# Kernel tuning notes

Measured on AMD Instinct MI355X. Metric: run time of the kernel, lower is better.

## Reference

```python
import jax, jax.numpy as jnp
import numpy as np

B, IN, H = 4096, 1024, 1024


def setup_inputs() -> dict:
    key = jax.random.key(0)
    k1, k2, k3, k4 = jax.random.split(key, 4)
    x = jax.random.normal(k1, (B, IN), dtype=jnp.float32)
    h_prev = jax.random.normal(k2, (B, H), dtype=jnp.float32)
    c_prev = jax.random.normal(k3, (B, H), dtype=jnp.float32)
    # Kaiming-uniform-ish init for W: bound = sqrt(6 / fan_in)
    fan_in = IN + H
    bound = np.sqrt(6.0 / fan_in)
    W = jax.random.uniform(k4, (4 * H, IN + H), dtype=jnp.float32,
                           minval=-bound, maxval=bound)
    # bias zero except forget-gate bias = 1.0 (first H entries)
    b = jnp.zeros((4 * H,), dtype=jnp.float32).at[:H].set(1.0)
    return {"x": x, "h_prev": h_prev, "c_prev": c_prev, "W": W, "b": b}


def reference(x, h_prev, c_prev, W, b):
    Hdim = c_prev.shape[1]
    combined = jnp.concatenate([x, h_prev], axis=1)        # (B, IN+H)
    gates = combined @ W.T + b                             # (B, 4H)
    f = jax.nn.sigmoid(gates[:, :Hdim])
    i = jax.nn.sigmoid(gates[:, Hdim:2 * Hdim])
    g = jnp.tanh(gates[:, 2 * Hdim:3 * Hdim])
    o = jax.nn.sigmoid(gates[:, 3 * Hdim:])
    c_t = f * c_prev + i * g
    h_t = o * jnp.tanh(c_t)
    return (h_t, c_t)
```

## Files before the change

### kernel.cpp

```cpp
#include <hip/hip_runtime.h>
#include <stdint.h>

#define Bn 4096
#define INn 1024
#define Hn 1024
#define Kn 2048
#define Nn 4096

#define BM 128
#define BK 64

typedef __attribute__((ext_vector_type(8))) short bf16x8;
typedef __attribute__((ext_vector_type(4))) float f32x4;
typedef __attribute__((ext_vector_type(4))) unsigned short us4;

__device__ __forceinline__ unsigned short f2bf(float f) {
  uint32_t u = __float_as_uint(f);
  u += 0x7fffu + ((u >> 16) & 1u);
  return (unsigned short)(u >> 16);
}

typedef __attribute__((address_space(3))) unsigned int as3_uint;
typedef const __attribute__((address_space(1))) unsigned int as1_uint;

__device__ __forceinline__ void gload16(const unsigned short* g, unsigned short* l) {
  __builtin_amdgcn_global_load_lds((as1_uint*)g, (as3_uint*)l, 16, 0, 0);
}

__device__ __forceinline__ float sigm(float x) { return 1.f / (1.f + __expf(-x)); }
__device__ __forceinline__ float tanh_fast(float x) { return 2.f / (1.f + __expf(-2.f * x)) - 1.f; }

__global__ void pack_bf16(const float* __restrict__ src, unsigned short* __restrict__ dst,
                          int log2cols, int dst_stride, int dst_col_off, long nquads) {
  long stride = (long)gridDim.x * blockDim.x;
  for (long q = (long)blockIdx.x * blockDim.x + threadIdx.x; q < nquads; q += stride) {
    long e = q << 2;
    int row = (int)(e >> log2cols);
    int col = (int)(e & ((1L << log2cols) - 1));
    float4 v = *(const float4*)(src + e);
    us4 o;
    o.x = f2bf(v.x); o.y = f2bf(v.y); o.z = f2bf(v.z); o.w = f2bf(v.w);
    *(us4*)(dst + (long)row * dst_stride + dst_col_off + col) = o;
  }
}

__global__ void lstm_gemm_fused(const unsigned short* __restrict__ A,
                                const unsigned short* __restrict__ Wbf,
                                const float* __restrict__ c_prev,
                                const float* __restrict__ bias,
                                float* __restrict__ out) {
  __shared__ unsigned short As[BM * BK];
  __shared__ unsigned short Bs[BM * BK];
  const int tid = threadIdx.x;
  const int lane = tid & 63;
  const int wid = tid >> 6;
  const int wr = wid >> 1;
  const int wc = wid & 1;
  const int brow = blockIdx.y * BM;
  const int h0 = blockIdx.x * 32;

  const int srow = tid >> 3;
  const int skoff = (tid & 7) * 8;

  const int l15 = lane & 15;
  const int lk = (lane >> 4) * 8;

  f32x4 acc[4][4] = {};

  for (int kt = 0; kt < Kn / BK; ++kt) {
    const int k0 = kt * BK;
#pragma unroll
    for (int i = 0; i < 4; ++i) {
      gload16(A + (long)(brow + i * 32 + srow) * Kn + k0 + skoff,
              &As[(i * 32 + srow) * BK + skoff]);
      const int rb = i * 32 + srow;
      const int grow = ((rb >> 4) & 3) * 1024 + h0 + ((rb >> 6) << 4) + (rb & 15);
      gload16(Wbf + (long)grow * Kn + k0 + skoff,
              &Bs[rb * BK + skoff]);
    }
    __syncthreads();
#pragma unroll
    for (int ks = 0; ks < 2; ++ks) {
      bf16x8 af[4], bfr[4];
#pragma unroll
      for (int m = 0; m < 4; ++m)
        af[m] = *(const bf16x8*)&As[(wr * 64 + m * 16 + l15) * BK + ks * 32 + lk];
#pragma unroll
      for (int n = 0; n < 4; ++n)
        bfr[n] = *(const bf16x8*)&Bs[(wc * 64 + n * 16 + l15) * BK + ks * 32 + lk];
#pragma unroll
      for (int m = 0; m < 4; ++m)
#pragma unroll
        for (int n = 0; n < 4; ++n)
          acc[m][n] = __builtin_amdgcn_mfma_f32_16x16x32_bf16(af[m], bfr[n], acc[m][n], 0, 0, 0);
    }
    __syncthreads();
  }

  const int hcol = h0 + wc * 16 + l15;
  const float bf_ = bias[hcol];
  const float bi_ = bias[1024 + hcol];
  const float bg_ = bias[2048 + hcol];
  const float bo_ = bias[3072 + hcol];
  const int rbase = brow + wr * 64 + ((lane >> 4) << 2);
  const long BH = (long)Bn * Hn;
#pragma unroll
  for (int m = 0; m < 4; ++m) {
#pragma unroll
    for (int j = 0; j < 4; ++j) {
      const long r = rbase + m * 16 + j;
      const float f = sigm(acc[m][0][j] + bf_);
      const float i_ = sigm(acc[m][1][j] + bi_);
      const float g = tanh_fast(acc[m][2][j] + bg_);
      const float o = sigm(acc[m][3][j] + bo_);
      const float cp = c_prev[r * Hn + hcol];
      const float ct = f * cp + i_ * g;
      const float ht = o * tanh_fast(ct);
      out[r * Hn + hcol] = ht;
      out[BH + r * Hn + hcol] = ct;
    }
  }
}

extern "C" void kernel_launch(void* const* d_in, const int* in_sizes, int n_in,
                              void* d_out, int out_size, void* d_ws, size_t ws_size,
                              hipStream_t stream) {
  const float* x      = (const float*)d_in[0];
  const float* h_prev = (const float*)d_in[1];
  const float* c_prev = (const float*)d_in[2];
  const float* W      = (const float*)d_in[3];
  const float* bias   = (const float*)d_in[4];
  float* out = (float*)d_out;

  unsigned short* Abf = (unsigned short*)d_ws;
  unsigned short* Wbf = Abf + (long)Bn * Kn;

  pack_bf16<<<2048, 256, 0, stream>>>(x, Abf, 10, Kn, 0, (long)Bn * INn / 4);
  pack_bf16<<<2048, 256, 0, stream>>>(h_prev, Abf, 10, Kn, INn, (long)Bn * Hn / 4);
  pack_bf16<<<2048, 256, 0, stream>>>(W, Wbf, 11, Kn, 0, (long)Nn * Kn / 4);

  dim3 grid(Hn / 32, Bn / BM);
  lstm_gemm_fused<<<grid, 256, 0, stream>>>(Abf, Wbf, c_prev, bias, out);
}
```

Before: 204.5 us.

## Triple-buffer GEMM with swizzled LDS, larger tile, and single fused pack kernel

Merges the three bf16 pack launches into one kernel. Rewrites the GEMM main loop to use a 3-stage LDS ring with async global-to-LDS loads and explicit vmcnt waits, so tile fetches overlap the MFMA work. It also XOR-swizzles the LDS layout to avoid bank conflicts, and doubles the N tile to 64 hidden columns with 512-thread blocks. Split barriers and s_setprio interleave loads with MFMAs, at the cost of more LDS per block and hand-tuned wait counts that must match the number of outstanding loads.

```diff
diff --git a/kernel.cpp b/kernel.cpp
--- a/kernel.cpp
+++ b/kernel.cpp
@@ -8,7 +8,9 @@
 #define Nn 4096
 
 #define BM 128
+#define BN 256
 #define BK 64
+#define KT (Kn / BK)
 
 typedef __attribute__((ext_vector_type(8))) short bf16x8;
 typedef __attribute__((ext_vector_type(4))) float f32x4;
@@ -30,78 +32,149 @@
 __device__ __forceinline__ float sigm(float x) { return 1.f / (1.f + __expf(-x)); }
 __device__ __forceinline__ float tanh_fast(float x) { return 2.f / (1.f + __expf(-2.f * x)) - 1.f; }
 
-__global__ void pack_bf16(const float* __restrict__ src, unsigned short* __restrict__ dst,
-                          int log2cols, int dst_stride, int dst_col_off, long nquads) {
-  long stride = (long)gridDim.x * blockDim.x;
-  for (long q = (long)blockIdx.x * blockDim.x + threadIdx.x; q < nquads; q += stride) {
-    long e = q << 2;
-    int row = (int)(e >> log2cols);
-    int col = (int)(e & ((1L << log2cols) - 1));
-    float4 v = *(const float4*)(src + e);
+__global__ void pack_all(const float* __restrict__ x, const float* __restrict__ h,
+                         const float* __restrict__ W,
+                         unsigned short* __restrict__ Abf, unsigned short* __restrict__ Wbf) {
+  const long XQ = (long)Bn * INn / 4;
+  const long WQ = (long)Nn * Kn / 4;
+  const long total = XQ + XQ + WQ;
+  const long stride = (long)gridDim.x * blockDim.x;
+  for (long q = (long)blockIdx.x * blockDim.x + threadIdx.x; q < total; q += stride) {
+    float4 v;
+    unsigned short* dst;
+    if (q < XQ) {
+      long e = q << 2;
+      v = *(const float4*)(x + e);
+      dst = Abf + ((long)(e >> 10) * Kn) + (e & 1023);
+    } else if (q < 2 * XQ) {
+      long e = (q - XQ) << 2;
+      v = *(const float4*)(h + e);
+      dst = Abf + ((long)(e >> 10) * Kn) + INn + (e & 1023);
+    } else {
+      long e = (q - 2 * XQ) << 2;
+      v = *(const float4*)(W + e);
+      dst = Wbf + e;
+    }
     us4 o;
     o.x = f2bf(v.x); o.y = f2bf(v.y); o.z = f2bf(v.z); o.w = f2bf(v.w);
-    *(us4*)(dst + (long)row * dst_stride + dst_col_off + col) = o;
+    *(us4*)dst = o;
   }
 }
 
-__global__ void lstm_gemm_fused(const unsigned short* __restrict__ A,
-                                const unsigned short* __restrict__ Wbf,
-                                const float* __restrict__ c_prev,
-                                const float* __restrict__ bias,
-                                float* __restrict__ out) {
-  __shared__ unsigned short As[BM * BK];
-  __shared__ unsigned short Bs[BM * BK];
+#define STAGE_A(t_, b_) do {                                                     \
+    const int k0_ = (t_) * BK;                                                   \
+    gload16(Ag + (long)(brow + srow) * Kn + k0_ + scol,                          \
+            &bufA[b_][srow * BK + sc8 * 8]);                                     \
+    gload16(Ag + (long)(brow + 64 + srow) * Kn + k0_ + scol,                     \
+            &bufA[b_][(64 + srow) * BK + sc8 * 8]);                              \
+  } while (0)
+#define STAGE_B(t_, b_, j_) do {                                                 \
+    const int k0_ = (t_) * BK;                                                   \
+    const int rb_ = (j_) * 64 + srow;                                            \
+    const int grow_ = ((rb_ >> 4) & 3) * Hn + h0 + ((rb_ >> 6) << 4) + (rb_ & 15);\
+    gload16(Wg + (long)grow_ * Kn + k0_ + scol,                                  \
+            &bufB[b_][rb_ * BK + sc8 * 8]);                                      \
+  } while (0)
+#define FENCE() do { asm volatile("" ::: "memory"); __builtin_amdgcn_sched_barrier(0); } while (0)
+
+__global__ void __launch_bounds__(512, 2)
+lstm_gemm_fused(const unsigned short* __restrict__ Ag,
+                const unsigned short* __restrict__ Wg,
+                const float* __restrict__ c_prev,
+                const float* __restrict__ bias,
+                float* __restrict__ out) {
+  __shared__ unsigned short bufA[3][BM * BK];
+  __shared__ unsigned short bufB[3][BN * BK];
+
   const int tid = threadIdx.x;
   const int lane = tid & 63;
   const int wid = tid >> 6;
-  const int wr = wid >> 1;
-  const int wc = wid & 1;
+  const int wr = wid >> 2;
+  const int wc = wid & 3;
   const int brow = blockIdx.y * BM;
-  const int h0 = blockIdx.x * 32;
+  const int h0 = blockIdx.x * 64;
 
   const int srow = tid >> 3;
-  const int skoff = (tid & 7) * 8;
+  const int sc8 = tid & 7;
+  const int scol = ((sc8 ^ (srow & 7)) * 8);
 
   const int l15 = lane & 15;
-  const int lk = (lane >> 4) * 8;
+  const int s7 = l15 & 7;
+  const int cA = lane >> 4;
+  const int aOff0 = (wr * 64 + l15) * BK + ((cA) ^ s7) * 8;
+  const int aOff1 = (wr * 64 + l15) * BK + ((cA + 4) ^ s7) * 8;
+  const int bOff0 = (wc * 64 + l15) * BK + ((cA) ^ s7) * 8;
+  const int bOff1 = (wc * 64 + l15) * BK + ((cA + 4) ^ s7) * 8;
 
   f32x4 acc[4][4] = {};
 
-  for (int kt = 0; kt < Kn / BK; ++kt) {
-    const int k0 = kt * BK;
-#pragma unroll
-    for (int i = 0; i < 4; ++i) {
-      gload16(A + (long)(brow + i * 32 + srow) * Kn + k0 + skoff,
-              &As[(i * 32 + srow) * BK + skoff]);
-      const int rb = i * 32 + srow;
-      const int grow = ((rb >> 4) & 3) * 1024 + h0 + ((rb >> 6) << 4) + (rb & 15);
-      gload16(Wbf + (long)grow * Kn + k0 + skoff,
-              &Bs[rb * BK + skoff]);
-    }
-    __syncthreads();
-#pragma unroll
-    for (int ks = 0; ks < 2; ++ks) {
-      bf16x8 af[4], bfr[4];
-#pragma unroll
-      for (int m = 0; m < 4; ++m)
-        af[m] = *(const bf16x8*)&As[(wr * 64 + m * 16 + l15) * BK + ks * 32 + lk];
-#pragma unroll
-      for (int n = 0; n < 4; ++n)
-        bfr[n] = *(const bf16x8*)&Bs[(wc * 64 + n * 16 + l15) * BK + ks * 32 + lk];
-#pragma unroll
-      for (int m = 0; m < 4; ++m)
-#pragma unroll
-        for (int n = 0; n < 4; ++n)
-          acc[m][n] = __builtin_amdgcn_mfma_f32_16x16x32_bf16(af[m], bfr[n], acc[m][n], 0, 0, 0);
-    }
-    __syncthreads();
+  STAGE_A(0, 0); STAGE_B(0, 0, 0); STAGE_B(0, 0, 1); STAGE_B(0, 0, 2); STAGE_B(0, 0, 3);
+  STAGE_A(1, 1); STAGE_B(1, 1, 0); STAGE_B(1, 1, 1); STAGE_B(1, 1, 2); STAGE_B(1, 1, 3);
+
+  for (int t = 0; t < KT; ++t) {
+    const int bi = t % 3;
+    const int sb = (t + 2) % 3;
+    const bool st = (t + 2) < KT;
+    if (t < KT - 1) asm volatile("s_waitcnt vmcnt(6)" ::: "memory");
+    else            asm volatile("s_waitcnt vmcnt(0)" ::: "memory");
+    __builtin_amdgcn_s_barrier();
+    FENCE();
+
+    const unsigned short* As = bufA[bi];
+    const unsigned short* Bs = bufB[bi];
+    bf16x8 bfr[4][2], af[2][2];
+
+#pragma unroll
+    for (int n = 0; n < 4; ++n) {
+      bfr[n][0] = *(const bf16x8*)&Bs[bOff0 + n * 16 * BK];
+      bfr[n][1] = *(const bf16x8*)&Bs[bOff1 + n * 16 * BK];
+    }
+#pragma unroll
+    for (int m = 0; m < 2; ++m) {
+      af[m][0] = *(const bf16x8*)&As[aOff0 + m * 16 * BK];
+      af[m][1] = *(const bf16x8*)&As[aOff1 + m * 16 * BK];
+    }
+    if (st) { STAGE_A(t + 2, sb); STAGE_B(t + 2, sb, 0); }
+    __builtin_amdgcn_s_barrier();
+    FENCE();
+    __builtin_amdgcn_s_setprio(1);
+#pragma unroll
+    for (int m = 0; m < 2; ++m)
+#pragma unroll
+      for (int n = 0; n < 4; ++n) {
+        acc[m][n] = __builtin_amdgcn_mfma_f32_16x16x32_bf16(af[m][0], bfr[n][0], acc[m][n], 0, 0, 0);
+        acc[m][n] = __builtin_amdgcn_mfma_f32_16x16x32_bf16(af[m][1], bfr[n][1], acc[m][n], 0, 0, 0);
+      }
+    __builtin_amdgcn_s_setprio(0);
+    FENCE();
+    __builtin_amdgcn_s_barrier();
+    FENCE();
+
+#pragma unroll
+    for (int m = 0; m < 2; ++m) {
+      af[m][0] = *(const bf16x8*)&As[aOff0 + (m + 2) * 16 * BK];
+      af[m][1] = *(const bf16x8*)&As[aOff1 + (m + 2) * 16 * BK];
+    }
+    if (st) { STAGE_B(t + 2, sb, 1); STAGE_B(t + 2, sb, 2); STAGE_B(t + 2, sb, 3); }
+    __builtin_amdgcn_s_barrier();
+    FENCE();
+    __builtin_amdgcn_s_setprio(1);
+#pragma unroll
+    for (int m = 0; m < 2; ++m)
+#pragma unroll
+      for (int n = 0; n < 4; ++n) {
+        acc[m + 2][n] = __builtin_amdgcn_mfma_f32_16x16x32_bf16(af[m][0], bfr[n][0], acc[m + 2][n], 0, 0, 0);
+        acc[m + 2][n] = __builtin_amdgcn_mfma_f32_16x16x32_bf16(af[m][1], bfr[n][1], acc[m + 2][n], 0, 0, 0);
+      }
+    __builtin_amdgcn_s_setprio(0);
+    FENCE();
   }
 
   const int hcol = h0 + wc * 16 + l15;
   const float bf_ = bias[hcol];
-  const float bi_ = bias[1024 + hcol];
-  const float bg_ = bias[2048 + hcol];
-  const float bo_ = bias[3072 + hcol];
+  const float bi_ = bias[Hn + hcol];
+  const float bg_ = bias[2 * Hn + hcol];
+  const float bo_ = bias[3 * Hn + hcol];
   const int rbase = brow + wr * 64 + ((lane >> 4) << 2);
   const long BH = (long)Bn * Hn;
 #pragma unroll
@@ -115,8 +188,7 @@
       const float o = sigm(acc[m][3][j] + bo_);
       const float cp = c_prev[r * Hn + hcol];
       const float ct = f * cp + i_ * g;
-      const float ht = o * tanh_fast(ct);
-      out[r * Hn + hcol] = ht;
+      out[r * Hn + hcol] = o * tanh_fast(ct);
       out[BH + r * Hn + hcol] = ct;
     }
   }
@@ -135,10 +207,8 @@
   unsigned short* Abf = (unsigned short*)d_ws;
   unsigned short* Wbf = Abf + (long)Bn * Kn;
 
-  pack_bf16<<<2048, 256, 0, stream>>>(x, Abf, 10, Kn, 0, (long)Bn * INn / 4);
-  pack_bf16<<<2048, 256, 0, stream>>>(h_prev, Abf, 10, Kn, INn, (long)Bn * Hn / 4);
-  pack_bf16<<<2048, 256, 0, stream>>>(W, Wbf, 11, Kn, 0, (long)Nn * Kn / 4);
-
-  dim3 grid(Hn / 32, Bn / BM);
-  lstm_gemm_fused<<<grid, 256, 0, stream>>>(Abf, Wbf, c_prev, bias, out);
-}
+  pack_all<<<2048, 256, 0, stream>>>(x, h_prev, W, Abf, Wbf);
+
+  dim3 grid(Hn / 64, Bn / BM);
+  lstm_gemm_fused<<<grid, 512, 0, stream>>>(Abf, Wbf, c_prev, bias, out);
+}
```

Result: slower. 223.6 us (+9.3%).
